# Performance work log

Measured on AMD Instinct MI355X. Metric: run time of the kernel, lower is better.

The kernel has to match this reference:

```python
import jax, jax.numpy as jnp
import numpy as np

B, H, W, DIM = 16, 28, 28, 256
HEADS, K = 8, 7
HD = DIM // HEADS
MLP = int(DIM * 4.0)
EPS = 1e-5


def setup_inputs() -> dict:
    key = jax.random.key(0)
    ks = jax.random.split(key, 8)
    s = 0.02
    return {
        "x": jax.random.normal(ks[0], (B, H, W, DIM), jnp.float32),
        "norm1_w": jnp.ones((DIM,), jnp.float32),
        "norm1_b": jnp.zeros((DIM,), jnp.float32),
        "qkv_w": jax.random.normal(ks[1], (3 * DIM, DIM), jnp.float32) * s,
        "qkv_b": jnp.zeros((3 * DIM,), jnp.float32),
        "rpb": jax.random.normal(ks[2], (HEADS, 2 * K - 1, 2 * K - 1), jnp.float32) * s,
        "proj_w": jax.random.normal(ks[3], (DIM, DIM), jnp.float32) * s,
        "proj_b": jnp.zeros((DIM,), jnp.float32),
        "norm2_w": jnp.ones((DIM,), jnp.float32),
        "norm2_b": jnp.zeros((DIM,), jnp.float32),
        "fc1_w": jax.random.normal(ks[4], (MLP, DIM), jnp.float32) * s,
        "fc1_b": jnp.zeros((MLP,), jnp.float32),
        "fc2_w": jax.random.normal(ks[5], (DIM, MLP), jnp.float32) * s,
        "fc2_b": jnp.zeros((DIM,), jnp.float32),
    }


def _ln(x, w, b):
    m = jnp.mean(x, axis=-1, keepdims=True)
    v = jnp.var(x, axis=-1, keepdims=True)  # biased, as torch LayerNorm
    return (x - m) * jax.lax.rsqrt(v + EPS) * w + b


def _window_idx(n):
    # NATTEN border handling: window shifts so every query has exactly K neighbors
    start = jnp.clip(jnp.arange(n) - K // 2, 0, n - K)  # [n]
    idx = start[:, None] + jnp.arange(K)                # [n, K] absolute neighbor index
    rel = idx - jnp.arange(n)[:, None] + (K - 1)        # [n, K] rpb index in [0, 2K-2]
    return idx, rel


def _neighborhood_attn(x, qkv_w, qkv_b, rpb, proj_w, proj_b):
    b, h, w, c = x.shape
    qkv = (x @ qkv_w.T + qkv_b).reshape(b, h, w, 3, HEADS, HD)
    q, k, v = qkv[:, :, :, 0], qkv[:, :, :, 1], qkv[:, :, :, 2]  # [b,h,w,heads,hd]
    q = q * (HD ** -0.5)
    idx_h, rel_h = _window_idx(h)
    idx_w, rel_w = _window_idx(w)
    # gather K/V neighborhoods: [b,h,K,w,K,heads,hd]
    kwin = k[:, idx_h][:, :, :, idx_w]
    vwin = v[:, idx_h][:, :, :, idx_w]
    # logits per query (i,j) over its KxK window
    attn = jnp.einsum('bijhd,biajchd->bhijac', q, kwin)  # [b,heads,h,w,K,K]
    bias = rpb[:, rel_h]                 # [heads,h,K,2K-1]
    bias = bias[:, :, :, rel_w]          # [heads,h,K,w,K]
    bias = bias.transpose(0, 1, 3, 2, 4) # [heads,h,w,K,K]
    attn = attn + bias[None]
    attn = jax.nn.softmax(attn.reshape(b, HEADS, h, w, K * K), axis=-1)
    attn = attn.reshape(b, HEADS, h, w, K, K)
    out = jnp.einsum('bhijac,biajchd->bijhd', attn, vwin).reshape(b, h, w, c)
    return out @ proj_w.T + proj_b


def reference(x, norm1_w, norm1_b, qkv_w, qkv_b, rpb, proj_w, proj_b,
              norm2_w, norm2_b, fc1_w, fc1_b, fc2_w, fc2_b):
    shortcut = x
    x = _ln(x, norm1_w, norm1_b)
    x = shortcut + _neighborhood_attn(x, qkv_w, qkv_b, rpb, proj_w, proj_b)
    h = _ln(x, norm2_w, norm2_b) @ fc1_w.T + fc1_b
    h = jax.nn.gelu(h, approximate=False)  # torch nn.GELU default (erf)
    return x + (h @ fc2_w.T + fc2_b)
```

## Files before the change

### kernel.cpp

```cpp
#include <hip/hip_runtime.h>
#include <hip/hip_bf16.h>
#include <math.h>

#define DIM   256
#define HEADS 8
#define HD    32
#define KW    7
#define HH    28
#define WW    28
#define BBATCH 16
#define NTOK  (BBATCH*HH*WW)
#define MLPD  1024
#define EPSLN 1e-5f
#define QSCALE 0.17677669529663687f

#define AS1 __attribute__((address_space(1)))
#define AS3 __attribute__((address_space(3)))

typedef __attribute__((ext_vector_type(8))) short short8;
typedef __attribute__((ext_vector_type(4))) float f32x4;
typedef unsigned short us;

__device__ __forceinline__ float b2f(us u) {
  union { float f; unsigned u; } x; x.u = ((unsigned)u) << 16; return x.f;
}
__device__ __forceinline__ us f2b(float f) {
  union { float f; unsigned u; } x; x.f = f;
  unsigned lsb = (x.u >> 16) & 1;
  x.u += 0x7fffu + lsb;
  return (us)(x.u >> 16);
}
__device__ __forceinline__ bool probe_f32(const us* p) { return p[0] == 0; }

__device__ __forceinline__ void gll16(const us* g, us* l) {
  __builtin_amdgcn_global_load_lds((const AS1 unsigned*)(const void*)g,
                                   (AS3 unsigned*)(void*)l, 16, 0, 0);
}

__device__ __forceinline__ float gelu_f(float x) {
  const float y = 0.7978845608028654f * x * (1.0f + 0.044715f * x * x);
  const float u = __expf(2.0f * y);
  const float th = 1.0f - 2.0f / (u + 1.0f);
  return 0.5f * x * (1.0f + th);
}

__global__ __launch_bounds__(256) void pre_kernel(const void* s0, const void* s1,
                                                  const void* s2, const void* s3,
                                                  us* d0, us* d1, us* d2, us* d3,
                                                  const void* p0, const void* p1, const void* p2,
                                                  const void* p3, const void* p4, const void* p5,
                                                  const void* p6, const void* p7, const void* p8,
                                                  float* __restrict__ pack,
                                                  const void* __restrict__ x,
                                                  us* __restrict__ xn1,
                                                  float* __restrict__ bias_t,
                                                  const us* __restrict__ probe)
{
  const bool isf32 = probe_f32(probe);
  const int blk = blockIdx.x;
  const int t = threadIdx.x;
  if (blk < 768) {
    const int gi = (blk * 256 + t) * 4;
    const void* src; us* dst; int loc; bool qs = false;
    if (gi < 196608)      { src = s0; dst = d0; loc = gi; qs = (loc < 65536); }
    else if (gi < 262144) { src = s1; dst = d1; loc = gi - 196608; }
    else if (gi < 524288) { src = s2; dst = d2; loc = gi - 262144; }
    else                  { src = s3; dst = d3; loc = gi - 524288; }
    float v[4];
    if (isf32) {
      const float4 f = *(const float4*)((const float*)src + loc);
      v[0] = f.x; v[1] = f.y; v[2] = f.z; v[3] = f.w;
    } else {
      ushort4 u = *(const ushort4*)((const us*)src + loc);
      v[0] = b2f(u.x); v[1] = b2f(u.y); v[2] = b2f(u.z); v[3] = b2f(u.w);
    }
    const float sc = qs ? QSCALE : 1.0f;
    ushort4 o;
    o.x = f2b(v[0] * sc); o.y = f2b(v[1] * sc); o.z = f2b(v[2] * sc); o.w = f2b(v[3] * sc);
    *(ushort4*)(dst + loc) = o;
  } else if (blk < 777) {
    const int seg = blk - 768;
    const void* srcs[9] = {p0, p1, p2, p3, p4, p5, p6, p7, p8};
    const int offs[9] = {0, 256, 512, 1280, 1536, 1792, 2048, 3072, 3328};
    const int lens[9] = {256, 256, 768, 256, 256, 256, 1024, 256, 1352};
    const void* s = srcs[seg];
    const int off = offs[seg], len = lens[seg];
    for (int i = t; i < len; i += 256) {
      float v = isf32 ? ((const float*)s)[i] : b2f(((const us*)s)[i]);
      if (seg == 2 && i < 256) v *= QSCALE;
      pack[off + i] = v;
    }
  } else if (blk < 3913) {
    const int wave = t >> 6, lane = t & 63;
    const int tok = (blk - 777) * 4 + wave;
    const int c0 = lane * 4;
    float v[4];
    if (isf32) {
      const float4 f = *(const float4*)((const float*)x + (size_t)tok * DIM + c0);
      v[0] = f.x; v[1] = f.y; v[2] = f.z; v[3] = f.w;
    } else {
      ushort4 u = *(const ushort4*)((const us*)x + (size_t)tok * DIM + c0);
      v[0] = b2f(u.x); v[1] = b2f(u.y); v[2] = b2f(u.z); v[3] = b2f(u.w);
    }
    float s  = v[0] + v[1] + v[2] + v[3];
    float s2 = v[0]*v[0] + v[1]*v[1] + v[2]*v[2] + v[3]*v[3];
    #pragma unroll
    for (int m = 32; m; m >>= 1) { s += __shfl_xor(s, m); s2 += __shfl_xor(s2, m); }
    const float mean = s * (1.0f / DIM);
    const float var  = s2 * (1.0f / DIM) - mean * mean;
    const float rstd = rsqrtf(var + EPSLN);
    float wv[4], bv[4];
    if (isf32) {
      const float4 a = *(const float4*)((const float*)p0 + c0);
      const float4 c = *(const float4*)((const float*)p1 + c0);
      wv[0]=a.x; wv[1]=a.y; wv[2]=a.z; wv[3]=a.w;
      bv[0]=c.x; bv[1]=c.y; bv[2]=c.z; bv[3]=c.w;
    } else {
      ushort4 a = *(const ushort4*)((const us*)p0 + c0);
      ushort4 c = *(const ushort4*)((const us*)p1 + c0);
      wv[0]=b2f(a.x); wv[1]=b2f(a.y); wv[2]=b2f(a.z); wv[3]=b2f(a.w);
      bv[0]=b2f(c.x); bv[1]=b2f(c.y); bv[2]=b2f(c.z); bv[3]=b2f(c.w);
    }
    ushort4 o;
    o.x = f2b((v[0] - mean) * rstd * wv[0] + bv[0]);
    o.y = f2b((v[1] - mean) * rstd * wv[1] + bv[1]);
    o.z = f2b((v[2] - mean) * rstd * wv[2] + bv[2]);
    o.w = f2b((v[3] - mean) * rstd * wv[3] + bv[3]);
    *(ushort4*)(xn1 + (size_t)tok * DIM + c0) = o;
  } else {
    const int ph = blk - 3913;
    const int p  = ph >> 3, h = ph & 7;
    const int i0 = 2 * p;
    const int si0 = min(max(i0 - 3, 0), 21);
    float* bt = bias_t + (size_t)ph * (224 * 64);
    for (int e = 0; e < 56; ++e) {
      const int idx = e * 256 + t;
      const int kv = idx >> 6;
      const int q  = idx & 63;
      const int isub = q >> 5;
      const int cq = q & 31;
      const int iq = i0 + isub;
      const int siq = min(max(iq - 3, 0), 21);
      const int sj  = min(max(cq - 3, 0), 21);
      const int rr  = (kv * 2341) >> 16;
      const int ar  = si0 + rr;
      const int ck  = kv - rr * 28;
      const int dr = ar - siq, dc = ck - sj;
      const bool valid = (cq < 28) && (dr >= 0) && (dr < 7) && (dc >= 0) && (dc < 7);
      float val = -1e30f;
      if (valid) {
        const int ridx = h * 169 + (ar - iq + 6) * 13 + (ck - cq + 6);
        val = isf32 ? ((const float*)p8)[ridx] : b2f(((const us*)p8)[ridx]);
      }
      bt[idx] = val;
    }
  }
}

__global__ __launch_bounds__(256) void ln_kernel(const us* __restrict__ in,
                                                 const float* __restrict__ w,
                                                 const float* __restrict__ b,
                                                 us* __restrict__ out)
{
  const int t = threadIdx.x;
  const int wave = t >> 6, lane = t & 63;
  const int tok = blockIdx.x * 4 + wave;
  const int c0 = lane * 4;
  ushort4 u = *(const ushort4*)(in + (size_t)tok * DIM + c0);
  float v[4] = {b2f(u.x), b2f(u.y), b2f(u.z), b2f(u.w)};
  float s  = v[0] + v[1] + v[2] + v[3];
  float s2 = v[0]*v[0] + v[1]*v[1] + v[2]*v[2] + v[3]*v[3];
  #pragma unroll
  for (int m = 32; m; m >>= 1) { s += __shfl_xor(s, m); s2 += __shfl_xor(s2, m); }
  const float mean = s * (1.0f / DIM);
  const float var  = s2 * (1.0f / DIM) - mean * mean;
  const float rstd = rsqrtf(var + EPSLN);
  const float4 wv = *(const float4*)(w + c0);
  const float4 bv = *(const float4*)(b + c0);
  ushort4 o;
  o.x = f2b((v[0] - mean) * rstd * wv.x + bv.x);
  o.y = f2b((v[1] - mean) * rstd * wv.y + bv.y);
  o.z = f2b((v[2] - mean) * rstd * wv.z + bv.z);
  o.w = f2b((v[3] - mean) * rstd * wv.w + bv.w);
  *(ushort4*)(out + (size_t)tok * DIM + c0) = o;
}

template<int BM, int MODE>
__global__ __launch_bounds__(256) void gemm_kernel(const us* __restrict__ A,
                                                   const us* __restrict__ W,
                                                   const float* __restrict__ bias,
                                                   const void* __restrict__ resid,
                                                   void* __restrict__ out,
                                                   int N, int K,
                                                   const us* __restrict__ probe)
{
  constexpr int BN = 64;
  constexpr int MF = BM / 32;
  constexpr int NF = 2;
  constexpr int AG = BM / 64;
  constexpr int TILEB = 2 * (BM + BN) * 64;
  constexpr int CSB = (MODE == 3) ? BM * BN * 4 : BM * BN * 2;
  constexpr int SMB = TILEB > CSB ? TILEB : CSB;
  __shared__ char smem[SMB];
  us* Asb = (us*)smem;
  us* Bsb = (us*)smem + 2 * BM * 32;

  const int t = threadIdx.x;
  const int wave = t >> 6, lane = t & 63;
  const int wm = wave >> 1, wn = wave & 1;
  const int m0 = blockIdx.x * BM;
  const int n0 = blockIdx.y * BN;
  const int lm = lane & 15;
  const int g  = lane >> 4;

  const int gc = t ^ ((t >> 3) & 7);
  const int srow = gc >> 2;
  const int scol = (gc & 3) * 8;
  const us* Ag = A + (size_t)(m0 + srow) * K + scol;
  const us* Bg = W + (size_t)(n0 + srow) * K + scol;

  const int NS = K >> 5;
  #pragma unroll
  for (int gr = 0; gr < AG; ++gr)
    gll16(Ag + (size_t)(gr * 64) * K, &Asb[gr * 2048 + t * 8]);
  gll16(Bg, &Bsb[t * 8]);

  f32x4 acc[MF][NF] = {};
  int cur = 0;
  for (int s = 0; s < NS; ++s) {
    __syncthreads();
    if (s + 1 < NS) {
      const int kk = (s + 1) << 5;
      #pragma unroll
      for (int gr = 0; gr < AG; ++gr)
        gll16(Ag + (size_t)(gr * 64) * K + kk, &Asb[(cur ^ 1) * BM * 32 + gr * 2048 + t * 8]);
      gll16(Bg + kk, &Bsb[(cur ^ 1) * 2048 + t * 8]);
    }
    short8 a[MF], b[NF];
    #pragma unroll
    for (int mf = 0; mf < MF; ++mf) {
      const int row = wm * (BM / 2) + mf * 16 + lm;
      const int c = (row & 63) * 4 + g;
      const int sl = c ^ ((c >> 3) & 7);
      a[mf] = *(const short8*)(const void*)&Asb[cur * BM * 32 + (row >> 6) * 2048 + sl * 8];
    }
    #pragma unroll
    for (int nf = 0; nf < NF; ++nf) {
      const int row = wn * 32 + nf * 16 + lm;
      const int c = row * 4 + g;
      const int sl = c ^ ((c >> 3) & 7);
      b[nf] = *(const short8*)(const void*)&Bsb[cur * 2048 + sl * 8];
    }
    #pragma unroll
    for (int mf = 0; mf < MF; ++mf) {
      #pragma unroll
      for (int nf = 0; nf < NF; ++nf)
        acc[mf][nf] = __builtin_amdgcn_mfma_f32_16x16x32_bf16(a[mf], b[nf], acc[mf][nf], 0, 0, 0);
    }
    cur ^= 1;
  }

  const bool isf32 = (MODE == 1 || MODE == 3) ? probe_f32(probe) : false;
  const int col = lm;
  const int rb  = g * 4;
  __syncthreads();

  if (MODE == 3 && isf32) {
    float* Cf = (float*)smem;
    #pragma unroll
    for (int mf = 0; mf < MF; ++mf) {
      #pragma unroll
      for (int nf = 0; nf < NF; ++nf) {
        const int n_loc = wn * 32 + nf * 16 + col;
        const float bv = bias[n0 + n_loc];
        #pragma unroll
        for (int j = 0; j < 4; ++j) {
          const int m_loc = wm * (BM / 2) + mf * 16 + rb + j;
          const size_t off = (size_t)(m0 + m_loc) * N + (n0 + n_loc);
          float v = acc[mf][nf][j] + bv + b2f(((const us*)resid)[off]);
          Cf[m_loc * BN + (n_loc ^ ((m_loc & 7) << 3))] = v;
        }
      }
    }
    __syncthreads();
    constexpr int CH = BM * BN / 4;
    #pragma unroll
    for (int it = 0; it < CH / 256; ++it) {
      const int id = it * 256 + t;
      const int m = id >> 4, c = id & 15;
      const float4 val = *(const float4*)&Cf[m * BN + ((c ^ ((m & 7) << 1)) * 4)];
      *(float4*)((float*)out + (size_t)(m0 + m) * N + n0 + c * 4) = val;
    }
  } else {
    us* Cs = (us*)smem;
    #pragma unroll
    for (int mf = 0; mf < MF; ++mf) {
      #pragma unroll
      for (int nf = 0; nf < NF; ++nf) {
        const int n_loc = wn * 32 + nf * 16 + col;
        const float bv = bias[n0 + n_loc];
        #pragma unroll
        for (int j = 0; j < 4; ++j) {
          const int m_loc = wm * (BM / 2) + mf * 16 + rb + j;
          const size_t off = (size_t)(m0 + m_loc) * N + (n0 + n_loc);
          float v = acc[mf][nf][j] + bv;
          if (MODE == 1) v += isf32 ? ((const float*)resid)[off] : b2f(((const us*)resid)[off]);
          else if (MODE == 2) v = gelu_f(v);
          else if (MODE == 3) v += b2f(((const us*)resid)[off]);
          Cs[m_loc * BN + (n_loc ^ ((m_loc & 7) << 3))] = f2b(v);
        }
      }
    }
    __syncthreads();
    constexpr int CH = BM * BN / 8;
    #pragma unroll
    for (int it = 0; it < CH / 256; ++it) {
      const int id = it * 256 + t;
      const int m = id >> 3, c = id & 7;
      const uint4 val = *(const uint4*)&Cs[m * BN + (c ^ (m & 7)) * 8];
      *(uint4*)((us*)out + (size_t)(m0 + m) * N + n0 + c * 8) = val;
    }
  }
}

__global__ __launch_bounds__(256) void attn_kernel(const us* __restrict__ qkv,
                                                   const float* __restrict__ bias_t,
                                                   us* __restrict__ out)
{
  __shared__ us K_lds[896 * 8];
  __shared__ us Vt_lds[32 * 232];
  __shared__ us P_lds[64 * 232];

  const int raw = blockIdx.x;
  const int bid = (raw & 7) * 224 + (raw >> 3);
  const int b  = bid & 15;
  const int ph = bid >> 4;
  const int p  = ph >> 3;
  const int h  = ph & 7;
  const int i0 = 2 * p;
  const int t = threadIdx.x;
  const int wave = t >> 6, lane = t & 63;
  const int lm = lane & 15, g = lane >> 4;
  const int kb = g * 8;
  const int si0 = min(max(i0 - 3, 0), 21);
  const int si1 = min(max(i0 - 2, 0), 21);
  const int nch = (si1 + 7 - si0) * 112;

  const us* kg = qkv + ((size_t)(b * 784 + si0 * 28)) * 768 + 256 + h * 32;
  const us* vg = kg + 256;

  const int c0 = t, c1 = 256 + t, c2 = 512 + t, c3 = 768 + t;
  const bool has3 = c3 < nch;
  uint4 v0 = *(const uint4*)(const void*)(vg + (size_t)(c0 >> 2) * 768 + (c0 & 3) * 8);
  uint4 v1 = *(const uint4*)(const void*)(vg + (size_t)(c1 >> 2) * 768 + (c1 & 3) * 8);
  uint4 v2 = *(const uint4*)(const void*)(vg + (size_t)(c2 >> 2) * 768 + (c2 & 3) * 8);
  uint4 v3;
  if (has3) v3 = *(const uint4*)(const void*)(vg + (size_t)(c3 >> 2) * 768 + (c3 & 3) * 8);

  {
    int gk;
    gk = c0 ^ ((c0 >> 3) & 7); gll16(kg + (size_t)(gk >> 2) * 768 + (gk & 3) * 8, &K_lds[c0 * 8]);
    gk = c1 ^ ((c1 >> 3) & 7); gll16(kg + (size_t)(gk >> 2) * 768 + (gk & 3) * 8, &K_lds[c1 * 8]);
    gk = c2 ^ ((c2 >> 3) & 7); gll16(kg + (size_t)(gk >> 2) * 768 + (gk & 3) * 8, &K_lds[c2 * 8]);
    if (has3) { gk = c3 ^ ((c3 >> 3) & 7); gll16(kg + (size_t)(gk >> 2) * 768 + (gk & 3) * 8, &K_lds[c3 * 8]); }
  }

  if (nch == 784) {
    if (t < 112) *(uint4*)(void*)&K_lds[(784 + t) * 8] = make_uint4(0, 0, 0, 0);
    const int ch = t >> 3, of = 196 + (t & 7) * 4;
    *(uint2*)(void*)&Vt_lds[ch * 232 + of] = make_uint2(0, 0);
  }

  {
    const unsigned uu0[4] = {v0.x, v0.y, v0.z, v0.w};
    const unsigned uu1[4] = {v1.x, v1.y, v1.z, v1.w};
    const unsigned uu2[4] = {v2.x, v2.y, v2.z, v2.w};
    #pragma unroll
    for (int e = 0; e < 4; ++e) {
      Vt_lds[((c0 & 3) * 8 + 2*e)     * 232 + (c0 >> 2)] = (us)(uu0[e] & 0xffffu);
      Vt_lds[((c0 & 3) * 8 + 2*e + 1) * 232 + (c0 >> 2)] = (us)(uu0[e] >> 16);
      Vt_lds[((c1 & 3) * 8 + 2*e)     * 232 + (c1 >> 2)] = (us)(uu1[e] & 0xffffu);
      Vt_lds[((c1 & 3) * 8 + 2*e + 1) * 232 + (c1 >> 2)] = (us)(uu1[e] >> 16);
      Vt_lds[((c2 & 3) * 8 + 2*e)     * 232 + (c2 >> 2)] = (us)(uu2[e] & 0xffffu);
      Vt_lds[((c2 & 3) * 8 + 2*e + 1) * 232 + (c2 >> 2)] = (us)(uu2[e] >> 16);
    }
    if (has3) {
      const unsigned uu3[4] = {v3.x, v3.y, v3.z, v3.w};
      #pragma unroll
      for (int e = 0; e < 4; ++e) {
        Vt_lds[((c3 & 3) * 8 + 2*e)     * 232 + (c3 >> 2)] = (us)(uu3[e] & 0xffffu);
        Vt_lds[((c3 & 3) * 8 + 2*e + 1) * 232 + (c3 >> 2)] = (us)(uu3[e] >> 16);
      }
    }
  }

  const int qcol_l = min((wave & 1) * 16 + lm, 27);
  const int iq = i0 + (wave >> 1);
  const short8 qa = *(const short8*)(const void*)(qkv + ((size_t)(b * 784 + iq * 28 + qcol_l)) * 768 + h * 32 + kb);

  __syncthreads();

  f32x4 s[14];
  #pragma unroll
  for (int n = 0; n < 14; ++n) {
    const int sl0 = (n * 16 + lm) * 4 + g;
    const int sl = sl0 ^ ((sl0 >> 3) & 7);
    const short8 kf = *(const short8*)(const void*)&K_lds[sl * 8];
    f32x4 z = {0.f, 0.f, 0.f, 0.f};
    s[n] = __builtin_amdgcn_mfma_f32_16x16x32_bf16(qa, kf, z, 0, 0, 0);
  }

  const float* bt = bias_t + (size_t)ph * (224 * 64);
  const int qb = wave * 16 + g * 4;
  float mx[4] = {-1e30f, -1e30f, -1e30f, -1e30f};
  #pragma unroll
  for (int n = 0; n < 14; ++n) {
    const f32x4 bb = *(const f32x4*)(const void*)&bt[(n * 16 + lm) * 64 + qb];
    #pragma unroll
    for (int jj = 0; jj < 4; ++jj) {
      const float r = s[n][jj] + bb[jj];
      s[n][jj] = r;
      mx[jj] = fmaxf(mx[jj], r);
    }
  }
  float sm[4];
  #pragma unroll
  for (int jj = 0; jj < 4; ++jj) {
    float m = mx[jj];
    m = fmaxf(m, __shfl_xor(m, 1)); m = fmaxf(m, __shfl_xor(m, 2));
    m = fmaxf(m, __shfl_xor(m, 4)); m = fmaxf(m, __shfl_xor(m, 8));
    float acc = 0.f;
    #pragma unroll
    for (int n = 0; n < 14; ++n) {
      const float e = __expf(s[n][jj] - m);
      acc += e;
      P_lds[(qb + jj) * 232 + n * 16 + lm] = f2b(e);
    }
    acc += __shfl_xor(acc, 1); acc += __shfl_xor(acc, 2);
    acc += __shfl_xor(acc, 4); acc += __shfl_xor(acc, 8);
    sm[jj] = acc;
  }

  #pragma unroll
  for (int nto = 0; nto < 2; ++nto) {
    f32x4 o = {0.f, 0.f, 0.f, 0.f};
    #pragma unroll
    for (int ks = 0; ks < 7; ++ks) {
      const short8 pa = *(const short8*)(const void*)&P_lds[(wave * 16 + lm) * 232 + ks * 32 + kb];
      const short8 vb = *(const short8*)(const void*)&Vt_lds[(nto * 16 + lm) * 232 + ks * 32 + kb];
      o = __builtin_amdgcn_mfma_f32_16x16x32_bf16(pa, vb, o, 0, 0, 0);
    }
    #pragma unroll
    for (int jj = 0; jj < 4; ++jj) {
      const int qc = (wave & 1) * 16 + g * 4 + jj;
      if (qc < 28) {
        const float inv = 1.0f / sm[jj];
        out[((size_t)(b * 784 + iq * 28 + qc)) * 256 + h * 32 + nto * 16 + lm] = f2b(o[jj] * inv);
      }
    }
  }
}

extern "C" void kernel_launch(void* const* d_in, const int* in_sizes, int n_in,
                              void* d_out, int out_size, void* d_ws, size_t ws_size,
                              hipStream_t stream)
{
  const us* probe = (const us*)d_in[1];

  char* ws = (char*)d_ws;
  us*    wqkv_c = (us*)(ws);
  us*    wproj_c= (us*)(ws + 393216);
  us*    wfc1_c = (us*)(ws + 524288);
  us*    wfc2_c = (us*)(ws + 1048576);
  float* pack   = (float*)(ws + 1572864);
  float* bias_t = (float*)(ws + 1593344);
  us*    xn1    = (us*)(ws + 8015872);
  us*    qkv    = (us*)(ws + 14438400);
  us*    out1   = (us*)(ws + 33705984);
  us*    hbuf   = (us*)(ws + 40128512);
  us*    att    = xn1;
  us*    xn2    = qkv;

  const float* p_qkvb = pack + 512;
  const float* p_projb= pack + 1280;
  const float* p_n2w  = pack + 1536;
  const float* p_n2b  = pack + 1792;
  const float* p_fc1b = pack + 2048;
  const float* p_fc2b = pack + 3072;

  pre_kernel<<<4025, 256, 0, stream>>>(d_in[3], d_in[6], d_in[10], d_in[12],
                                       wqkv_c, wproj_c, wfc1_c, wfc2_c,
                                       d_in[1], d_in[2], d_in[4], d_in[7], d_in[8], d_in[9],
                                       d_in[11], d_in[13], d_in[5], pack,
                                       d_in[0], xn1, bias_t, probe);
  gemm_kernel<128, 0><<<dim3(NTOK / 128, 768 / 64), 256, 0, stream>>>(xn1, wqkv_c, p_qkvb, nullptr, qkv, 768, 256, probe);
  attn_kernel<<<BBATCH * (HH / 2) * HEADS, 256, 0, stream>>>(qkv, bias_t, att);
  gemm_kernel<64, 1><<<dim3(NTOK / 64, DIM / 64), 256, 0, stream>>>(att, wproj_c, p_projb, d_in[0], out1, DIM, 256, probe);
  ln_kernel<<<NTOK / 4, 256, 0, stream>>>(out1, p_n2w, p_n2b, xn2);
  gemm_kernel<128, 2><<<dim3(NTOK / 128, MLPD / 64), 256, 0, stream>>>(xn2, wfc1_c, p_fc1b, nullptr, hbuf, MLPD, 256, probe);
  gemm_kernel<64, 3><<<dim3(NTOK / 64, DIM / 64), 256, 0, stream>>>(hbuf, wfc2_c, p_fc2b, out1, d_out, DIM, MLPD, probe);
}
```

Measured before the change: 123.1 us.

## Store attention bias in bf16, alias K/P LDS, and parametrize GEMM K-tile

The relative-position bias table is now written and read as bf16 instead of fp32, halving the bytes the attention kernel reads for it. The attention kernel reuses one LDS buffer for K and for the softmax probabilities, with an added barrier, which lowers LDS use per block and may raise occupancy. The GEMM gets a BK template parameter with generalized staging, and the proj and fc2 GEMMs use BK=64 to halve the number of k-step barriers. The cost is bf16 rounding of the bias and more LDS per GEMM block at the larger tile.

```diff
diff --git a/kernel.cpp b/kernel.cpp
--- a/kernel.cpp
+++ b/kernel.cpp
@@ -53,7 +53,7 @@
                                                   float* __restrict__ pack,
                                                   const void* __restrict__ x,
                                                   us* __restrict__ xn1,
-                                                  float* __restrict__ bias_t,
+                                                  us* __restrict__ bias_t,
                                                   const us* __restrict__ probe)
 {
   const bool isf32 = probe_f32(probe);
@@ -132,7 +132,7 @@
     const int p  = ph >> 3, h = ph & 7;
     const int i0 = 2 * p;
     const int si0 = min(max(i0 - 3, 0), 21);
-    float* bt = bias_t + (size_t)ph * (224 * 64);
+    us* bt = bias_t + (size_t)ph * (224 * 64);
     for (int e = 0; e < 56; ++e) {
       const int idx = e * 256 + t;
       const int kv = idx >> 6;
@@ -152,7 +152,7 @@
         const int ridx = h * 169 + (ar - iq + 6) * 13 + (ck - cq + 6);
         val = isf32 ? ((const float*)p8)[ridx] : b2f(((const us*)p8)[ridx]);
       }
-      bt[idx] = val;
+      bt[idx] = f2b(val);
     }
   }
 }
@@ -185,7 +185,7 @@
   *(ushort4*)(out + (size_t)tok * DIM + c0) = o;
 }
 
-template<int BM, int MODE>
+template<int BM, int BK, int MODE>
 __global__ __launch_bounds__(256) void gemm_kernel(const us* __restrict__ A,
                                                    const us* __restrict__ W,
                                                    const float* __restrict__ bias,
@@ -197,13 +197,17 @@
   constexpr int BN = 64;
   constexpr int MF = BM / 32;
   constexpr int NF = 2;
-  constexpr int AG = BM / 64;
-  constexpr int TILEB = 2 * (BM + BN) * 64;
-  constexpr int CSB = (MODE == 3) ? BM * BN * 4 : BM * BN * 2;
+  constexpr int CPR = BK / 8;
+  constexpr int ACH = BM * CPR;
+  constexpr int BCH = BN * CPR;
+  constexpr int ASZ = BM * BK;
+  constexpr int BSZ = BN * BK;
+  constexpr int TILEB = 2 * (ASZ + BSZ) * 2;
+  constexpr int CSB = BM * BN * 4;
   constexpr int SMB = TILEB > CSB ? TILEB : CSB;
   __shared__ char smem[SMB];
   us* Asb = (us*)smem;
-  us* Bsb = (us*)smem + 2 * BM * 32;
+  us* Bsb = (us*)smem + 2 * ASZ;
 
   const int t = threadIdx.x;
   const int wave = t >> 6, lane = t & 63;
@@ -213,52 +217,60 @@
   const int lm = lane & 15;
   const int g  = lane >> 4;
 
-  const int gc = t ^ ((t >> 3) & 7);
-  const int srow = gc >> 2;
-  const int scol = (gc & 3) * 8;
-  const us* Ag = A + (size_t)(m0 + srow) * K + scol;
-  const us* Bg = W + (size_t)(n0 + srow) * K + scol;
-
-  const int NS = K >> 5;
-  #pragma unroll
-  for (int gr = 0; gr < AG; ++gr)
-    gll16(Ag + (size_t)(gr * 64) * K, &Asb[gr * 2048 + t * 8]);
-  gll16(Bg, &Bsb[t * 8]);
+  const int NS = K / BK;
+
+  #define STAGE(buf, kk)                                                         \
+    {                                                                            \
+      _Pragma("unroll")                                                          \
+      for (int i = 0; i < ACH / 256; ++i) {                                      \
+        const int slot = i * 256 + t;                                            \
+        const int gc = slot ^ ((slot >> 3) & 7);                                 \
+        gll16(A + (size_t)(m0 + gc / CPR) * K + (kk) + (gc % CPR) * 8,           \
+              &Asb[(buf) * ASZ + slot * 8]);                                     \
+      }                                                                          \
+      _Pragma("unroll")                                                          \
+      for (int i = 0; i < BCH / 256; ++i) {                                      \
+        const int slot = i * 256 + t;                                            \
+        const int gc = slot ^ ((slot >> 3) & 7);                                 \
+        gll16(W + (size_t)(n0 + gc / CPR) * K + (kk) + (gc % CPR) * 8,           \
+              &Bsb[(buf) * BSZ + slot * 8]);                                     \
+      }                                                                          \
+    }
+
+  STAGE(0, 0);
 
   f32x4 acc[MF][NF] = {};
   int cur = 0;
   for (int s = 0; s < NS; ++s) {
     __syncthreads();
-    if (s + 1 < NS) {
-      const int kk = (s + 1) << 5;
+    if (s + 1 < NS) STAGE(cur ^ 1, (s + 1) * BK);
+    #pragma unroll
+    for (int kh = 0; kh < BK / 32; ++kh) {
+      short8 a[MF], b[NF];
       #pragma unroll
-      for (int gr = 0; gr < AG; ++gr)
-        gll16(Ag + (size_t)(gr * 64) * K + kk, &Asb[(cur ^ 1) * BM * 32 + gr * 2048 + t * 8]);
-      gll16(Bg + kk, &Bsb[(cur ^ 1) * 2048 + t * 8]);
-    }
-    short8 a[MF], b[NF];
-    #pragma unroll
-    for (int mf = 0; mf < MF; ++mf) {
-      const int row = wm * (BM / 2) + mf * 16 + lm;
-      const int c = (row & 63) * 4 + g;
-      const int sl = c ^ ((c >> 3) & 7);
-      a[mf] = *(const short8*)(const void*)&Asb[cur * BM * 32 + (row >> 6) * 2048 + sl * 8];
-    }
-    #pragma unroll
-    for (int nf = 0; nf < NF; ++nf) {
-      const int row = wn * 32 + nf * 16 + lm;
-      const int c = row * 4 + g;
-      const int sl = c ^ ((c >> 3) & 7);
-      b[nf] = *(const short8*)(const void*)&Bsb[cur * 2048 + sl * 8];
-    }
-    #pragma unroll
-    for (int mf = 0; mf < MF; ++mf) {
+      for (int mf = 0; mf < MF; ++mf) {
+        const int row = wm * (BM / 2) + mf * 16 + lm;
+        const int c = row * CPR + kh * 4 + g;
+        const int sl = c ^ ((c >> 3) & 7);
+        a[mf] = *(const short8*)(const void*)&Asb[cur * ASZ + sl * 8];
+      }
       #pragma unroll
-      for (int nf = 0; nf < NF; ++nf)
-        acc[mf][nf] = __builtin_amdgcn_mfma_f32_16x16x32_bf16(a[mf], b[nf], acc[mf][nf], 0, 0, 0);
+      for (int nf = 0; nf < NF; ++nf) {
+        const int row = wn * 32 + nf * 16 + lm;
+        const int c = row * CPR + kh * 4 + g;
+        const int sl = c ^ ((c >> 3) & 7);
+        b[nf] = *(const short8*)(const void*)&Bsb[cur * BSZ + sl * 8];
+      }
+      #pragma unroll
+      for (int mf = 0; mf < MF; ++mf) {
+        #pragma unroll
+        for (int nf = 0; nf < NF; ++nf)
+          acc[mf][nf] = __builtin_amdgcn_mfma_f32_16x16x32_bf16(a[mf], b[nf], acc[mf][nf], 0, 0, 0);
+      }
     }
     cur ^= 1;
   }
+  #undef STAGE
 
   const bool isf32 = (MODE == 1 || MODE == 3) ? probe_f32(probe) : false;
   const int col = lm;
@@ -324,12 +336,11 @@
 }
 
 __global__ __launch_bounds__(256) void attn_kernel(const us* __restrict__ qkv,
-                                                   const float* __restrict__ bias_t,
+                                                   const us* __restrict__ bias_t,
                                                    us* __restrict__ out)
 {
-  __shared__ us K_lds[896 * 8];
+  __shared__ us KP_lds[64 * 232];
   __shared__ us Vt_lds[32 * 232];
-  __shared__ us P_lds[64 * 232];
 
   const int raw = blockIdx.x;
   const int bid = (raw & 7) * 224 + (raw >> 3);
@@ -359,16 +370,16 @@
 
   {
     int gk;
-    gk = c0 ^ ((c0 >> 3) & 7); gll16(kg + (size_t)(gk >> 2) * 768 + (gk & 3) * 8, &K_lds[c0 * 8]);
-    gk = c1 ^ ((c1 >> 3) & 7); gll16(kg + (size_t)(gk >> 2) * 768 + (gk & 3) * 8, &K_lds[c1 * 8]);
-    gk = c2 ^ ((c2 >> 3) & 7); gll16(kg + (size_t)(gk >> 2) * 768 + (gk & 3) * 8, &K_lds[c2 * 8]);
-    if (has3) { gk = c3 ^ ((c3 >> 3) & 7); gll16(kg + (size_t)(gk >> 2) * 768 + (gk & 3) * 8, &K_lds[c3 * 8]); }
+    gk = c0 ^ ((c0 >> 3) & 7); gll16(kg + (size_t)(gk >> 2) * 768 + (gk & 3) * 8, &KP_lds[c0 * 8]);
+    gk = c1 ^ ((c1 >> 3) & 7); gll16(kg + (size_t)(gk >> 2) * 768 + (gk & 3) * 8, &KP_lds[c1 * 8]);
+    gk = c2 ^ ((c2 >> 3) & 7); gll16(kg + (size_t)(gk >> 2) * 768 + (gk & 3) * 8, &KP_lds[c2 * 8]);
+    if (has3) { gk = c3 ^ ((c3 >> 3) & 7); gll16(kg + (size_t)(gk >> 2) * 768 + (gk & 3) * 8, &KP_lds[c3 * 8]); }
   }
 
   if (nch == 784) {
-    if (t < 112) *(uint4*)(void*)&K_lds[(784 + t) * 8] = make_uint4(0, 0, 0, 0);
-    const int ch = t >> 3, of = 196 + (t & 7) * 4;
-    *(uint2*)(void*)&Vt_lds[ch * 232 + of] = make_uint2(0, 0);
+    if (t < 112) *(uint4*)(void*)&KP_lds[(784 + t) * 8] = make_uint4(0, 0, 0, 0);
+    const int ch = t & 31, slot = t >> 5;
+    *(uint2*)(void*)&Vt_lds[ch * 232 + 196 + slot * 4] = make_uint2(0, 0);
   }
 
   {
@@ -405,20 +416,23 @@
   for (int n = 0; n < 14; ++n) {
     const int sl0 = (n * 16 + lm) * 4 + g;
     const int sl = sl0 ^ ((sl0 >> 3) & 7);
-    const short8 kf = *(const short8*)(const void*)&K_lds[sl * 8];
+    const short8 kf = *(const short8*)(const void*)&KP_lds[sl * 8];
     f32x4 z = {0.f, 0.f, 0.f, 0.f};
     s[n] = __builtin_amdgcn_mfma_f32_16x16x32_bf16(qa, kf, z, 0, 0, 0);
   }
 
-  const float* bt = bias_t + (size_t)ph * (224 * 64);
+  __syncthreads();
+
+  const us* bt = bias_t + (size_t)ph * (224 * 64);
   const int qb = wave * 16 + g * 4;
   float mx[4] = {-1e30f, -1e30f, -1e30f, -1e30f};
   #pragma unroll
   for (int n = 0; n < 14; ++n) {
-    const f32x4 bb = *(const f32x4*)(const void*)&bt[(n * 16 + lm) * 64 + qb];
+    const ushort4 bb = *(const ushort4*)(const void*)&bt[(n * 16 + lm) * 64 + qb];
+    const float bbf[4] = {b2f(bb.x), b2f(bb.y), b2f(bb.z), b2f(bb.w)};
     #pragma unroll
     for (int jj = 0; jj < 4; ++jj) {
-      const float r = s[n][jj] + bb[jj];
+      const float r = s[n][jj] + bbf[jj];
       s[n][jj] = r;
       mx[jj] = fmaxf(mx[jj], r);
     }
@@ -434,7 +448,7 @@
     for (int n = 0; n < 14; ++n) {
       const float e = __expf(s[n][jj] - m);
       acc += e;
-      P_lds[(qb + jj) * 232 + n * 16 + lm] = f2b(e);
+      KP_lds[(qb + jj) * 232 + n * 16 + lm] = f2b(e);
     }
     acc += __shfl_xor(acc, 1); acc += __shfl_xor(acc, 2);
     acc += __shfl_xor(acc, 4); acc += __shfl_xor(acc, 8);
@@ -446,7 +460,7 @@
     f32x4 o = {0.f, 0.f, 0.f, 0.f};
     #pragma unroll
     for (int ks = 0; ks < 7; ++ks) {
-      const short8 pa = *(const short8*)(const void*)&P_lds[(wave * 16 + lm) * 232 + ks * 32 + kb];
+      const short8 pa = *(const short8*)(const void*)&KP_lds[(wave * 16 + lm) * 232 + ks * 32 + kb];
       const short8 vb = *(const short8*)(const void*)&Vt_lds[(nto * 16 + lm) * 232 + ks * 32 + kb];
       o = __builtin_amdgcn_mfma_f32_16x16x32_bf16(pa, vb, o, 0, 0, 0);
     }
@@ -473,7 +487,7 @@
   us*    wfc1_c = (us*)(ws + 524288);
   us*    wfc2_c = (us*)(ws + 1048576);
   float* pack   = (float*)(ws + 1572864);
-  float* bias_t = (float*)(ws + 1593344);
+  us*    bias_t = (us*)(ws + 1593344);
   us*    xn1    = (us*)(ws + 8015872);
   us*    qkv    = (us*)(ws + 14438400);
   us*    out1   = (us*)(ws + 33705984);
@@ -493,10 +507,10 @@
                                        d_in[1], d_in[2], d_in[4], d_in[7], d_in[8], d_in[9],
                                        d_in[11], d_in[13], d_in[5], pack,
                                        d_in[0], xn1, bias_t, probe);
-  gemm_kernel<128, 0><<<dim3(NTOK / 128, 768 / 64), 256, 0, stream>>>(xn1, wqkv_c, p_qkvb, nullptr, qkv, 768, 256, probe);
+  gemm_kernel<128, 32, 0><<<dim3(NTOK / 128, 768 / 64), 256, 0, stream>>>(xn1, wqkv_c, p_qkvb, nullptr, qkv, 768, 256, probe);
   attn_kernel<<<BBATCH * (HH / 2) * HEADS, 256, 0, stream>>>(qkv, bias_t, att);
-  gemm_kernel<64, 1><<<dim3(NTOK / 64, DIM / 64), 256, 0, stream>>>(att, wproj_c, p_projb, d_in[0], out1, DIM, 256, probe);
+  gemm_kernel<64, 64, 1><<<dim3(NTOK / 64, DIM / 64), 256, 0, stream>>>(att, wproj_c, p_projb, d_in[0], out1, DIM, 256, probe);
   ln_kernel<<<NTOK / 4, 256, 0, stream>>>(out1, p_n2w, p_n2b, xn2);
-  gemm_kernel<128, 2><<<dim3(NTOK / 128, MLPD / 64), 256, 0, stream>>>(xn2, wfc1_c, p_fc1b, nullptr, hbuf, MLPD, 256, probe);
-  gemm_kernel<64, 3><<<dim3(NTOK / 64, DIM / 64), 256, 0, stream>>>(hbuf, wfc2_c, p_fc2b, out1, d_out, DIM, MLPD, probe);
-}
+  gemm_kernel<128, 32, 2><<<dim3(NTOK / 128, MLPD / 64), 256, 0, stream>>>(xn2, wfc1_c, p_fc1b, nullptr, hbuf, MLPD, 256, probe);
+  gemm_kernel<64, 64, 3><<<dim3(NTOK / 64, DIM / 64), 256, 0, stream>>>(hbuf, wfc2_c, p_fc2b, out1, d_out, DIM, MLPD, probe);
+}
```

After: 118.8 us. 1.04x faster.
